# Optimization experiments

Measured on AMD Instinct MI355X. Metric: run time of the kernel, lower is better.

The kernel has to match this reference:

```python
import jax, jax.numpy as jnp
from jax import lax
import numpy as np


def _bn(x, g, b, eps=1e-5):
    # BatchNorm2d in training mode: biased batch stats over (N,H,W) per channel
    m = jnp.mean(x, axis=(0, 2, 3), keepdims=True)
    v = jnp.mean((x - m) ** 2, axis=(0, 2, 3), keepdims=True)
    return (x - m) * lax.rsqrt(v + eps) * g[None, :, None, None] + b[None, :, None, None]


def _conv(x, w, b, pad):
    y = lax.conv_general_dilated(x, w, (1, 1), [(pad, pad), (pad, pad)],
                                 dimension_numbers=('NCHW', 'OIHW', 'NCHW'))
    return y + b[None, :, None, None]


def _prelu(x, a):
    return jnp.where(x >= 0, x, a * x)


def _maxpool2(x):
    return lax.reduce_window(x, -jnp.inf, lax.max, (1, 1, 2, 2), (1, 1, 2, 2), 'VALID')


def _up2(x):
    # UpsamplingBilinear2d(scale_factor=2) -> bilinear, align_corners=True
    B, C, H, W = x.shape
    def idx(n):
        pos = jnp.arange(2 * n, dtype=x.dtype) * (n - 1) / (2 * n - 1)
        lo = jnp.floor(pos).astype(jnp.int32)
        hi = jnp.minimum(lo + 1, n - 1)
        return lo, hi, pos - lo.astype(x.dtype)
    lo, hi, f = idx(H)
    x = x[:, :, lo, :] * (1 - f)[:, None] + x[:, :, hi, :] * f[:, None]
    lo, hi, f = idx(W)
    x = x[:, :, :, lo] * (1 - f) + x[:, :, :, hi] * f
    return x


def _forward(x, n16, sigma16, bias16, prelu_a,
             bn3_g, bn3_b, bn32_g, bn32_b, bn64_g, bn64_b, bn128_g, bn128_b,
             w1, b1, w2, b2, w3, b3, w4, b4, w5, b5, w6, b6, w7, b7, w11, b11):
    B, C, H, W = x.shape
    # 16 enhancement curves fused: r_k = x^{n_k} / (x^{n_k} + sigma_k^{n_k} + bias_k)
    xn = x[None] ** n16[:, None, None, None, None]          # (16,B,3,H,W)
    r = xn / (xn + (sigma16 ** n16)[:, None, None, None, None]
              + bias16[:, None, None, None, None])
    # each branch gets its own BatchNorm2d(3) stats (same affine params)
    r = jax.vmap(lambda t: _bn(t, bn3_g, bn3_b))(r)
    x_fusion = jnp.transpose(r, (1, 0, 2, 3, 4)).reshape(B, 16 * C, H, W)
    x1 = _bn(_maxpool2(_prelu(_conv(x_fusion, w1, b1, 1), prelu_a)), bn32_g, bn32_b)
    x2 = _bn(_maxpool2(_prelu(_conv(x1, w2, b2, 1), prelu_a)), bn64_g, bn64_b)
    x3 = _bn(_maxpool2(_prelu(_conv(x2, w3, b3, 1), prelu_a)), bn128_g, bn128_b)
    x4 = _bn(_conv(x3, w4, b4, 1), bn128_g, bn128_b)
    x5 = _bn(_up2(_prelu(_conv(jnp.concatenate([x4, x3], 1), w5, b5, 1), prelu_a)), bn64_g, bn64_b)
    x6 = _bn(_up2(_prelu(_conv(jnp.concatenate([x2, x5], 1), w6, b6, 1), prelu_a)), bn32_g, bn32_b)
    x_out = jax.nn.sigmoid(_up2(_prelu(_conv(jnp.concatenate([x1, x6], 1), w7, b7, 1), prelu_a)))
    x_out = _conv(x_out, w11, b11, 0)
    x_mean = jnp.mean(x, axis=1, keepdims=True)
    x_out1 = jnp.mean(x_out, axis=1, keepdims=True)
    return x_out1 * (x / (x_mean + 1e-6))


def setup_inputs() -> dict:
    key = jax.random.key(0)
    ks = jax.random.split(key, 16)
    B, H, W = 8, 256, 256
    nf = 32
    x = jax.random.uniform(ks[0], (B, 3, H, W), jnp.float32, 1e-3, 1.0)
    n16 = jnp.arange(1, 17, dtype=jnp.float32) * 0.5
    sigma16 = jnp.full((16,), 0.5, jnp.float32)
    bias16 = jnp.full((16,), 1e-4, jnp.float32)
    prelu_a = jnp.float32(0.25)
    def cw(k, o, i, kk):
        return jax.random.normal(k, (o, i, kk, kk), jnp.float32) * 0.05
    def cb(o):
        return jnp.zeros((o,), jnp.float32)
    return dict(
        x=x, n16=n16, sigma16=sigma16, bias16=bias16, prelu_a=prelu_a,
        bn3_g=jnp.ones((3,), jnp.float32), bn3_b=jnp.zeros((3,), jnp.float32),
        bn32_g=jnp.ones((32,), jnp.float32), bn32_b=jnp.zeros((32,), jnp.float32),
        bn64_g=jnp.ones((64,), jnp.float32), bn64_b=jnp.zeros((64,), jnp.float32),
        bn128_g=jnp.ones((128,), jnp.float32), bn128_b=jnp.zeros((128,), jnp.float32),
        w1=cw(ks[1], nf, 48, 3), b1=cb(nf),
        w2=cw(ks[2], 2 * nf, nf, 3), b2=cb(2 * nf),
        w3=cw(ks[3], 4 * nf, 2 * nf, 3), b3=cb(4 * nf),
        w4=cw(ks[4], 4 * nf, 4 * nf, 3), b4=cb(4 * nf),
        w5=cw(ks[5], 2 * nf, 8 * nf, 3), b5=cb(2 * nf),
        w6=cw(ks[6], nf, 4 * nf, 3), b6=cb(nf),
        w7=cw(ks[7], nf, 2 * nf, 3), b7=cb(nf),
        w11=cw(ks[8], 3, nf, 1), b11=cb(3),
    )


def reference(x, n16, sigma16, bias16, prelu_a,
              bn3_g, bn3_b, bn32_g, bn32_b, bn64_g, bn64_b, bn128_g, bn128_b,
              w1, b1, w2, b2, w3, b3, w4, b4, w5, b5, w6, b6, w7, b7, w11, b11):
    return _forward(x, n16, sigma16, bias16, prelu_a,
                    bn3_g, bn3_b, bn32_g, bn32_b, bn64_g, bn64_b, bn128_g, bn128_b,
                    w1, b1, w2, b2, w3, b3, w4, b4, w5, b5, w6, b6, w7, b7, w11, b11)
```

## Files before the change

kernel.cpp:

```cpp
#include <hip/hip_runtime.h>

#define FAST_EXP2(x) __builtin_amdgcn_exp2f(x)
#define FAST_LOG2(x) __builtin_amdgcn_logf(x)
#define FAST_RCP(x)  __builtin_amdgcn_rcpf(x)

static constexpr size_t S3_SUM=0,   S3_SQ=48;
static constexpr size_t S32A_SUM=96,  S32A_SQ=128;
static constexpr size_t S64A_SUM=160, S64A_SQ=224;
static constexpr size_t S128A_SUM=288,S128A_SQ=416;
static constexpr size_t S128B_SUM=544,S128B_SQ=672;
static constexpr size_t S64B_SUM=800, S64B_SQ=864;
static constexpr size_t S32B_SUM=928, S32B_SQ=960;
static constexpr size_t A3_=1024,  B3_=1072;
static constexpr size_t A32A_=1120, B32A_=1152;
static constexpr size_t A64A_=1184, B64A_=1248;
static constexpr size_t A128A_=1312,B128A_=1440;
static constexpr size_t A128B_=1568,B128B_=1696;
static constexpr size_t A64B_=1824, B64B_=1888;
static constexpr size_t A32B_=1952, B32B_=1984;
static constexpr size_t SPB_=2016, WBAR_=2032, BBAR_=2064;
static constexpr size_t T1_=4096;
static constexpr size_t T2_=T1_+4194304;
static constexpr size_t T3_=T2_+2097152;
static constexpr size_t T4_=T3_+1048576;
static constexpr size_t C5_=T4_+1048576;
static constexpr size_t U5_=C5_+524288;
static constexpr size_t C6_=U5_+2097152;
static constexpr size_t U6_=C6_+1048576;
static constexpr size_t C7_=U6_+4194304;

__global__ void k_precomp(const float* __restrict__ n16, const float* __restrict__ sig16,
                          const float* __restrict__ b16, const float* __restrict__ w11,
                          const float* __restrict__ b11,
                          float* __restrict__ spb, float* __restrict__ wbar, float* __restrict__ bbar)
{
    int t = threadIdx.x;
    if (t < 16) spb[t] = powf(sig16[t], n16[t]) + b16[t];
    else if (t < 48) { int j = t - 16; wbar[j] = (w11[j] + w11[32 + j] + w11[64 + j]) * (1.f/3.f); }
    else if (t == 48) bbar[0] = (b11[0] + b11[1] + b11[2]) * (1.f/3.f);
}

__global__ __launch_bounds__(256) void k_branch_stats(
    const float* __restrict__ x, const float* __restrict__ n16,
    const float* __restrict__ sig16, const float* __restrict__ b16,
    float* __restrict__ sum, float* __restrict__ sq)
{
    const int c = blockIdx.x >> 6;
    const int chunk = blockIdx.x & 63;
    float nk[16], den[16];
#pragma unroll
    for (int k = 0; k < 16; ++k) { nk[k] = n16[k]; den[k] = powf(sig16[k], nk[k]) + b16[k]; }
    float s[16], q[16];
#pragma unroll
    for (int k = 0; k < 16; ++k) { s[k] = 0.f; q[k] = 0.f; }
    const int per = 8192;
    int start = chunk * per;
    for (int i = start + (int)threadIdx.x; i < start + per; i += 256) {
        int b = i >> 16, hw = i & 65535;
        float xv = x[(size_t)(b*3 + c)*65536 + hw];
        float t = FAST_LOG2(xv);
#pragma unroll
        for (int k = 0; k < 16; ++k) {
            float v = FAST_EXP2(nk[k]*t);
            float r = v * FAST_RCP(v + den[k]);
            s[k] += r; q[k] += r*r;
        }
    }
    __shared__ float red[4][32];
    int lane = threadIdx.x & 63, wid = threadIdx.x >> 6;
#pragma unroll
    for (int k = 0; k < 16; ++k) {
#pragma unroll
        for (int off = 32; off > 0; off >>= 1) {
            s[k] += __shfl_down(s[k], off);
            q[k] += __shfl_down(q[k], off);
        }
    }
    if (lane == 0) {
#pragma unroll
        for (int k = 0; k < 16; ++k) { red[wid][k] = s[k]; red[wid][16+k] = q[k]; }
    }
    __syncthreads();
    if (threadIdx.x < 32) {
        float v = red[0][threadIdx.x] + red[1][threadIdx.x] + red[2][threadIdx.x] + red[3][threadIdx.x];
        int k = threadIdx.x & 15;
        if (threadIdx.x < 16) atomicAdd(&sum[k*3 + c], v);
        else                  atomicAdd(&sq[k*3 + c], v);
    }
}

__global__ __launch_bounds__(256) void k_stats(
    const float* __restrict__ in, int C, int HW, int nchunks, int per,
    float* __restrict__ sum, float* __restrict__ sq)
{
    int c = blockIdx.x / nchunks;
    int chunk = blockIdx.x - c*nchunks;
    float s = 0.f, q = 0.f;
    int start = chunk * per, end = start + per;
    for (int i = start + (int)threadIdx.x; i < end; i += 256) {
        int b = i / HW, hw = i - b*HW;
        float v = in[((size_t)b*C + c)*HW + hw];
        s += v; q += v*v;
    }
#pragma unroll
    for (int off = 32; off > 0; off >>= 1) { s += __shfl_down(s, off); q += __shfl_down(q, off); }
    __shared__ float ss[4], qq[4];
    int lane = threadIdx.x & 63, wid = threadIdx.x >> 6;
    if (lane == 0) { ss[wid] = s; qq[wid] = q; }
    __syncthreads();
    if (threadIdx.x == 0) {
        atomicAdd(&sum[c], ss[0]+ss[1]+ss[2]+ss[3]);
        atomicAdd(&sq[c],  qq[0]+qq[1]+qq[2]+qq[3]);
    }
}

__global__ void k_finalize(const float* __restrict__ sum, const float* __restrict__ sq,
                           const float* __restrict__ g, const float* __restrict__ bb,
                           int C, int gdim, float invN,
                           float* __restrict__ A, float* __restrict__ Bs)
{
    int i = blockIdx.x*blockDim.x + threadIdx.x;
    if (i < C) {
        float m   = sum[i]*invN;
        float var = fmaxf(sq[i]*invN - m*m, 0.f);
        float inv = rsqrtf(var + 1e-5f);
        float a   = g[i % gdim]*inv;
        A[i]  = a;
        Bs[i] = bb[i % gdim] - m*a;
    }
}

__global__ __launch_bounds__(256) void k_fill(
    float* __restrict__ out, const float* __restrict__ bias, int C, int HW, int total)
{
    int idx = blockIdx.x*256 + threadIdx.x;
    if (idx < total) {
        int c = (idx / HW) % C;
        out[idx] = bias[c];
    }
}

template<int COG>
__device__ inline void stats_reduce8(float (&ssum)[COG], float (&ssq)[COG],
                                     float (*redst)[16], int cob,
                                     float* __restrict__ gsum, float* __restrict__ gsq)
{
    int lane = threadIdx.x & 63, wid = threadIdx.x >> 6;
#pragma unroll
    for (int co = 0; co < COG; ++co) {
#pragma unroll
        for (int off = 32; off > 0; off >>= 1) {
            ssum[co] += __shfl_down(ssum[co], off);
            ssq[co]  += __shfl_down(ssq[co],  off);
        }
    }
    if (lane == 0) {
#pragma unroll
        for (int co = 0; co < COG; ++co) { redst[wid][co] = ssum[co]; redst[wid][8+co] = ssq[co]; }
    }
    __syncthreads();
    if (threadIdx.x < 16) {
        float v = redst[0][threadIdx.x] + redst[1][threadIdx.x] + redst[2][threadIdx.x] + redst[3][threadIdx.x];
        if (threadIdx.x < 8) atomicAdd(&gsum[cob + threadIdx.x], v);
        else                 atomicAdd(&gsq[cob + threadIdx.x - 8], v);
    }
}

template<int COG>
__global__ __launch_bounds__(256,2) void k_conv1f(
    const float* __restrict__ x,
    const float* __restrict__ n16, const float* __restrict__ spb,
    const float* __restrict__ A, const float* __restrict__ Bs,
    const float* __restrict__ w, const float* __restrict__ bias,
    const float* __restrict__ prelu_a,
    float* __restrict__ out, float* __restrict__ gsum, float* __restrict__ gsq)
{
    const int tx = threadIdx.x & 15, ty = threadIdx.x >> 4;
    const int nco = 32 / COG;
    const int b = blockIdx.z / nco, cob = (blockIdx.z - b*nco)*COG;
    const int x0 = blockIdx.x*32, y0 = blockIdx.y*32;

    __shared__ float wl[COG*48*9];
    __shared__ float rl[3*1224];
    __shared__ float al[48], bl[48], nl[16], dl[16];
    __shared__ float redst[4][16];

    for (int t = threadIdx.x; t < COG*48*9; t += 256) {
        int co = t % COG; int rest = t / COG;
        int kk = rest % 9; int ci = rest / 9;
        wl[t] = w[(((size_t)(cob+co))*48 + ci)*9 + kk];
    }
    if (threadIdx.x < 48) { al[threadIdx.x] = A[threadIdx.x]; bl[threadIdx.x] = Bs[threadIdx.x]; }
    else if (threadIdx.x < 64)  nl[threadIdx.x-48] = n16[threadIdx.x-48];
    else if (threadIdx.x < 80)  dl[threadIdx.x-64] = spb[threadIdx.x-64];

    float tlr[14];
    int off_[14]; int chpack = 0; int okf = 0;
#pragma unroll
    for (int j = 0; j < 14; ++j) {
        int i = threadIdx.x + 256*j;
        if (i < 3468) {
            int ch = i / 1156, jj = i - ch*1156;
            int rr = jj / 34, cc = jj - rr*34;
            int gy = y0 - 1 + rr, gx = x0 - 1 + cc;
            bool ok = (unsigned)gy < 256u && (unsigned)gx < 256u;
            off_[j] = ch*1224 + rr*36 + cc;
            chpack |= ch << (2*j);
            tlr[j] = 0.f;
            if (ok) {
                okf |= 1 << j;
                tlr[j] = FAST_LOG2(x[((size_t)(b*3+ch))*65536 + gy*256 + gx]);
            }
        } else { off_[j] = 3671; tlr[j] = 0.f; }
    }

    float acc[COG][4];
#pragma unroll
    for (int i = 0; i < COG; ++i)
#pragma unroll
        for (int j = 0; j < 4; ++j) acc[i][j] = 0.f;

#pragma unroll 1
    for (int k = 0; k < 16; ++k) {
        __syncthreads();
        float nk = nl[k], dk = dl[k];
#pragma unroll
        for (int j = 0; j < 14; ++j) {
            float rv = 0.f;
            if (okf & (1 << j)) {
                int ch = (chpack >> (2*j)) & 3;
                int chg = k*3 + ch;
                float v = FAST_EXP2(nk * tlr[j]);
                rv = v * FAST_RCP(v + dk) * al[chg] + bl[chg];
            }
            rl[off_[j]] = rv;
        }
        __syncthreads();
#pragma unroll
        for (int ch = 0; ch < 3; ++ch) {
            const float* tlp = &rl[ch*1224 + (2*ty)*36 + 2*tx];
            float iv[4][4];
#pragma unroll
            for (int r = 0; r < 4; ++r) {
                float2 a2 = *(const float2*)(tlp + r*36);
                float2 b2 = *(const float2*)(tlp + r*36 + 2);
                iv[r][0]=a2.x; iv[r][1]=a2.y; iv[r][2]=b2.x; iv[r][3]=b2.y;
            }
            const float* wbase = &wl[((k*3+ch)*9)*COG];
#pragma unroll
            for (int kh = 0; kh < 3; ++kh)
#pragma unroll
            for (int kw = 0; kw < 3; ++kw) {
                const int kk = kh*3 + kw;
                float wv[COG];
#pragma unroll
                for (int q = 0; q < COG/4; ++q) {
                    float4 wq = *((const float4*)(wbase + kk*COG) + q);
                    wv[4*q+0]=wq.x; wv[4*q+1]=wq.y; wv[4*q+2]=wq.z; wv[4*q+3]=wq.w;
                }
#pragma unroll
                for (int co = 0; co < COG; ++co)
#pragma unroll
                    for (int py = 0; py < 2; ++py)
#pragma unroll
                        for (int px = 0; px < 2; ++px)
                            acc[co][py*2+px] += wv[co]*iv[py+kh][px+kw];
            }
        }
    }

    float a = __ldg(prelu_a);
    int pyp = (y0 >> 1) + ty, pxp = (x0 >> 1) + tx;
    float ssum[COG], ssq[COG];
#pragma unroll
    for (int co = 0; co < COG; ++co) {
        float bv = bias[cob + co];
        float v0 = acc[co][0] + bv, v1 = acc[co][1] + bv;
        float v2 = acc[co][2] + bv, v3 = acc[co][3] + bv;
        v0 = v0 >= 0.f ? v0 : a*v0; v1 = v1 >= 0.f ? v1 : a*v1;
        v2 = v2 >= 0.f ? v2 : a*v2; v3 = v3 >= 0.f ? v3 : a*v3;
        float m = fmaxf(fmaxf(v0,v1), fmaxf(v2,v3));
        out[(((size_t)b*32 + cob + co)*128 + pyp)*128 + pxp] = m;
        ssum[co] = m; ssq[co] = m*m;
    }
    __syncthreads();
    stats_reduce8<COG>(ssum, ssq, redst, cob, gsum, gsq);
}

template<int COG, bool POOL>
__global__ __launch_bounds__(256,2) void k_conv_big(
    const float* __restrict__ in1, int C1,
    const float* __restrict__ sc1, const float* __restrict__ sh1,
    const float* __restrict__ w, const float* __restrict__ bias,
    int Cout, int H, int W, const float* __restrict__ prelu_a, int do_prelu,
    float* __restrict__ out, float* __restrict__ gsum, float* __restrict__ gsq)
{
    const int Cin = C1;
    const int tx = threadIdx.x & 15, ty = threadIdx.x >> 4;
    const int nco = Cout / COG;
    const int b = blockIdx.z / nco, cob = (blockIdx.z - b*nco)*COG;
    const int x0 = blockIdx.x*64, y0 = blockIdx.y*32;

    __shared__ float wl[COG*64*9];
    __shared__ float tile[2][34*68];
    __shared__ float redst[4][16];

    for (int t = threadIdx.x; t < COG*Cin*9; t += 256) {
        int co = t % COG; int rest = t / COG;
        int k = rest % 9; int ci = rest / 9;
        wl[t] = w[(((size_t)(cob+co))*Cin + ci)*9 + k];
    }

    float acc[COG][8];
#pragma unroll
    for (int i = 0; i < COG; ++i)
#pragma unroll
        for (int j = 0; j < 8; ++j) acc[i][j] = 0.f;

#pragma unroll 1
    for (int cb = 0; cb < Cin; cb += 2) {
#pragma unroll
        for (int sub = 0; sub < 2; ++sub) {
            int ci = cb + sub;
            float scv = sc1 ? sc1[ci] : 1.f;
            float shv = sc1 ? sh1[ci] : 0.f;
            const float* base = in1 + ((size_t)b*Cin + ci)*H*W;
#pragma unroll 1
            for (int i = threadIdx.x; i < 34*66; i += 256) {
                int r = i / 66, c = i - r*66;
                int gy = y0 - 1 + r, gx = x0 - 1 + c;
                float v = 0.f;
                if ((unsigned)gy < (unsigned)H && (unsigned)gx < (unsigned)W)
                    v = base[(size_t)gy*W + gx]*scv + shv;
                tile[sub][r*68 + c] = v;
            }
        }
        __syncthreads();
#pragma unroll
        for (int sub = 0; sub < 2; ++sub) {
            const float* tl = &tile[sub][(2*ty)*68 + 4*tx];
            float iv[4][6];
#pragma unroll
            for (int r = 0; r < 4; ++r) {
                float4 av = *(const float4*)(tl + r*68);
                float2 bv = *(const float2*)(tl + r*68 + 4);
                iv[r][0]=av.x; iv[r][1]=av.y; iv[r][2]=av.z; iv[r][3]=av.w;
                iv[r][4]=bv.x; iv[r][5]=bv.y;
            }
            const float* wbase = &wl[(cb+sub)*9*COG];
#pragma unroll
            for (int kh = 0; kh < 3; ++kh)
#pragma unroll
            for (int kw = 0; kw < 3; ++kw) {
                const int k = kh*3 + kw;
                float wv[COG];
#pragma unroll
                for (int q = 0; q < COG/4; ++q) {
                    float4 wq = *((const float4*)(wbase + k*COG) + q);
                    wv[4*q+0]=wq.x; wv[4*q+1]=wq.y; wv[4*q+2]=wq.z; wv[4*q+3]=wq.w;
                }
#pragma unroll
                for (int co = 0; co < COG; ++co)
#pragma unroll
                    for (int py = 0; py < 2; ++py)
#pragma unroll
                        for (int px = 0; px < 4; ++px)
                            acc[co][py*4+px] += wv[co]*iv[py+kh][px+kw];
            }
        }
        __syncthreads();
    }

    float a = __ldg(prelu_a);
    float ssum[COG], ssq[COG];
    if (POOL) {
        const int Hp = H >> 1, Wp = W >> 1;
        int pyp = (y0 >> 1) + ty, pxp = (x0 >> 1) + 2*tx;
#pragma unroll
        for (int co = 0; co < COG; ++co) {
            float bv = bias[cob + co];
            float v[8];
#pragma unroll
            for (int p = 0; p < 8; ++p) {
                float t = acc[co][p] + bv;
                v[p] = t >= 0.f ? t : a*t;
            }
            float2 st;
            st.x = fmaxf(fmaxf(v[0], v[1]), fmaxf(v[4], v[5]));
            st.y = fmaxf(fmaxf(v[2], v[3]), fmaxf(v[6], v[7]));
            *(float2*)(out + (((size_t)b*Cout + cob + co)*Hp + pyp)*Wp + pxp) = st;
            ssum[co] = st.x + st.y; ssq[co] = st.x*st.x + st.y*st.y;
        }
        stats_reduce8<COG>(ssum, ssq, redst, cob, gsum, gsq);
    } else {
        int oy = y0 + 2*ty, ox = x0 + 4*tx;
#pragma unroll
        for (int co = 0; co < COG; ++co) {
            float bv = bias[cob + co];
            float* op = out + (((size_t)b*Cout + cob + co)*H + oy)*W + ox;
#pragma unroll
            for (int py = 0; py < 2; ++py) {
                float4 st;
                float t0 = acc[co][py*4+0] + bv, t1 = acc[co][py*4+1] + bv;
                float t2 = acc[co][py*4+2] + bv, t3 = acc[co][py*4+3] + bv;
                if (do_prelu) {
                    t0 = t0 >= 0.f ? t0 : a*t0; t1 = t1 >= 0.f ? t1 : a*t1;
                    t2 = t2 >= 0.f ? t2 : a*t2; t3 = t3 >= 0.f ? t3 : a*t3;
                }
                st.x=t0; st.y=t1; st.z=t2; st.w=t3;
                *(float4*)(op + py*W) = st;
            }
        }
    }
}

template<int COG, int MAXCI, bool POOL, bool SPLIT, bool STATS>
__global__ __launch_bounds__(256,2) void k_conv32(
    const float* __restrict__ in1, int C1,
    const float* __restrict__ sc1, const float* __restrict__ sh1,
    const float* __restrict__ in2, int C2,
    const float* __restrict__ sc2, const float* __restrict__ sh2,
    const float* __restrict__ w, const float* __restrict__ bias,
    int Cout, int H, int W, const float* __restrict__ prelu_a, int do_prelu,
    int ciN, int nsplit,
    float* __restrict__ out, float* __restrict__ gsum, float* __restrict__ gsq)
{
    const int Cin = C1 + C2;
    const int tx = threadIdx.x & 15, ty = threadIdx.x >> 4;
    const int nco = Cout / COG;
    int z = blockIdx.z;
    const int sp = z % nsplit; z /= nsplit;
    const int b = z / nco, cob = (z - b*nco)*COG;
    const int ci0 = sp * ciN;
    const int x0 = blockIdx.x*32, y0 = blockIdx.y*32;

    __shared__ float wl[COG*MAXCI*9];
    __shared__ float tile[2][34*36];
    __shared__ float redst[4][16];

    for (int t = threadIdx.x; t < COG*ciN*9; t += 256) {
        int co = t % COG; int rest = t / COG;
        int k = rest % 9; int ci = rest / 9;
        wl[t] = w[(((size_t)(cob+co))*Cin + ci0 + ci)*9 + k];
    }

    float acc[COG][4];
#pragma unroll
    for (int i = 0; i < COG; ++i)
#pragma unroll
        for (int j = 0; j < 4; ++j) acc[i][j] = 0.f;

#pragma unroll 1
    for (int cb = 0; cb < ciN; cb += 2) {
#pragma unroll
        for (int sub = 0; sub < 2; ++sub) {
            int ci = ci0 + cb + sub;
            const float* in; int cc; const float* scp; const float* shp; int Cn;
            if (ci < C1) { in = in1; cc = ci;      scp = sc1; shp = sh1; Cn = C1; }
            else         { in = in2; cc = ci - C1; scp = sc2; shp = sh2; Cn = C2; }
            float scv = scp ? scp[cc] : 1.f;
            float shv = scp ? shp[cc] : 0.f;
            const float* base = in + ((size_t)b*Cn + cc)*H*W;
#pragma unroll 1
            for (int i = threadIdx.x; i < 34*34; i += 256) {
                int r = i / 34, c = i - r*34;
                int gy = y0 - 1 + r, gx = x0 - 1 + c;
                float v = 0.f;
                if ((unsigned)gy < (unsigned)H && (unsigned)gx < (unsigned)W)
                    v = base[(size_t)gy*W + gx]*scv + shv;
                tile[sub][r*36 + c] = v;
            }
        }
        __syncthreads();
#pragma unroll
        for (int sub = 0; sub < 2; ++sub) {
            const float* tl = &tile[sub][(2*ty)*36 + 2*tx];
            float iv[4][4];
#pragma unroll
            for (int r = 0; r < 4; ++r) {
                float2 a2 = *(const float2*)(tl + r*36);
                float2 b2 = *(const float2*)(tl + r*36 + 2);
                iv[r][0]=a2.x; iv[r][1]=a2.y; iv[r][2]=b2.x; iv[r][3]=b2.y;
            }
            const float* wbase = &wl[(cb+sub)*9*COG];
#pragma unroll
            for (int kh = 0; kh < 3; ++kh)
#pragma unroll
            for (int kw = 0; kw < 3; ++kw) {
                const int k = kh*3 + kw;
                float wv[COG];
#pragma unroll
                for (int q = 0; q < COG/4; ++q) {
                    float4 wq = *((const float4*)(wbase + k*COG) + q);
                    wv[4*q+0]=wq.x; wv[4*q+1]=wq.y; wv[4*q+2]=wq.z; wv[4*q+3]=wq.w;
                }
#pragma unroll
                for (int co = 0; co < COG; ++co)
#pragma unroll
                    for (int py = 0; py < 2; ++py)
#pragma unroll
                        for (int px = 0; px < 2; ++px)
                            acc[co][py*2+px] += wv[co]*iv[py+kh][px+kw];
            }
        }
        __syncthreads();
    }

    if (SPLIT) {
        int oy = y0 + 2*ty, ox = x0 + 2*tx;
#pragma unroll
        for (int co = 0; co < COG; ++co) {
            float* op = out + (((size_t)b*Cout + cob + co)*H + oy)*W + ox;
            atomicAdd(&op[0],     acc[co][0]);
            atomicAdd(&op[1],     acc[co][1]);
            atomicAdd(&op[W],     acc[co][2]);
            atomicAdd(&op[W + 1], acc[co][3]);
        }
    } else {
        float a = __ldg(prelu_a);
        float ssum[COG], ssq[COG];
        if (POOL) {
            const int Hp = H >> 1, Wp = W >> 1;
            int pyp = (y0 >> 1) + ty, pxp = (x0 >> 1) + tx;
#pragma unroll
            for (int co = 0; co < COG; ++co) {
                float bv = bias[cob + co];
                float v0 = acc[co][0] + bv, v1 = acc[co][1] + bv;
                float v2 = acc[co][2] + bv, v3 = acc[co][3] + bv;
                v0 = v0 >= 0.f ? v0 : a*v0; v1 = v1 >= 0.f ? v1 : a*v1;
                v2 = v2 >= 0.f ? v2 : a*v2; v3 = v3 >= 0.f ? v3 : a*v3;
                float m = fmaxf(fmaxf(v0,v1), fmaxf(v2,v3));
                out[(((size_t)b*Cout + cob + co)*Hp + pyp)*Wp + pxp] = m;
                ssum[co] = m; ssq[co] = m*m;
            }
            if (STATS) stats_reduce8<COG>(ssum, ssq, redst, cob, gsum, gsq);
        } else {
            int oy = y0 + 2*ty, ox = x0 + 2*tx;
#pragma unroll
            for (int co = 0; co < COG; ++co) {
                float bv = bias[cob + co];
                float* op = out + (((size_t)b*Cout + cob + co)*H + oy)*W + ox;
                float v0 = acc[co][0] + bv, v1 = acc[co][1] + bv;
                float v2 = acc[co][2] + bv, v3 = acc[co][3] + bv;
                if (do_prelu) {
                    v0 = v0 >= 0.f ? v0 : a*v0; v1 = v1 >= 0.f ? v1 : a*v1;
                    v2 = v2 >= 0.f ? v2 : a*v2; v3 = v3 >= 0.f ? v3 : a*v3;
                }
                op[0] = v0; op[1] = v1; op[W] = v2; op[W+1] = v3;
                ssum[co] = v0+v1+v2+v3; ssq[co] = v0*v0+v1*v1+v2*v2+v3*v3;
            }
            if (STATS) stats_reduce8<COG>(ssum, ssq, redst, cob, gsum, gsq);
        }
    }
}

__global__ __launch_bounds__(256) void k_up2(
    const float* __restrict__ in, float* __restrict__ out, int C, int h, int w,
    const float* __restrict__ prelu_a, int do_prelu,
    float* __restrict__ gsum, float* __restrict__ gsq)
{
    int idx = blockIdx.x*256 + threadIdx.x;
    int W2 = 2*w, H2 = 2*h;
    float a = do_prelu ? __ldg(prelu_a) : 0.f;
    int ox = idx % W2; int t = idx / W2; int oy = t % H2; int bc = t / H2;
    float py = ((float)oy * (float)(h-1)) / (float)(2*h - 1);
    int ly = (int)floorf(py); int hy = min(ly+1, h-1); float fy = py - (float)ly;
    float px = ((float)ox * (float)(w-1)) / (float)(2*w - 1);
    int lx = (int)floorf(px); int hx = min(lx+1, w-1); float fx = px - (float)lx;
    const float* p = in + (size_t)bc*h*w;
    float v00 = p[(size_t)ly*w + lx], v01 = p[(size_t)ly*w + hx];
    float v10 = p[(size_t)hy*w + lx], v11 = p[(size_t)hy*w + hx];
    if (do_prelu) {
        v00 = v00 >= 0.f ? v00 : a*v00;
        v01 = v01 >= 0.f ? v01 : a*v01;
        v10 = v10 >= 0.f ? v10 : a*v10;
        v11 = v11 >= 0.f ? v11 : a*v11;
    }
    float v0 = v00*(1.f-fx) + v01*fx;
    float v1 = v10*(1.f-fx) + v11*fx;
    float v = v0*(1.f-fy) + v1*fy;
    out[idx] = v;
    float s = v, q = v*v;
#pragma unroll
    for (int off = 32; off > 0; off >>= 1) { s += __shfl_down(s, off); q += __shfl_down(q, off); }
    __shared__ float ss[4], qq[4];
    int lane = threadIdx.x & 63, wid = threadIdx.x >> 6;
    if (lane == 0) { ss[wid] = s; qq[wid] = q; }
    __syncthreads();
    if (threadIdx.x == 0) {
        int c = bc % C;
        atomicAdd(&gsum[c], ss[0]+ss[1]+ss[2]+ss[3]);
        atomicAdd(&gsq[c],  qq[0]+qq[1]+qq[2]+qq[3]);
    }
}

__global__ __launch_bounds__(256) void k_final(
    const float* __restrict__ c7, const float* __restrict__ x,
    const float* __restrict__ wbar, const float* __restrict__ bbar,
    float* __restrict__ out)
{
    int idx = blockIdx.x*256 + threadIdx.x;
    if (idx >= 8*65536) return;
    int hw = idx & 65535, b = idx >> 16;
    int oy = hw >> 8, ox = hw & 255;
    float py = ((float)oy * 127.f) / 255.f;
    int ly = (int)floorf(py); int hy = min(ly+1, 127); float fy = py - (float)ly;
    float px = ((float)ox * 127.f) / 255.f;
    int lx = (int)floorf(px); int hx = min(lx+1, 127); float fx = px - (float)lx;
    float w00 = (1.f-fy)*(1.f-fx), w01 = (1.f-fy)*fx, w10 = fy*(1.f-fx), w11v = fy*fx;
    const float* base = c7 + (size_t)b*32*16384;
    float accum = bbar[0];
#pragma unroll 8
    for (int j = 0; j < 32; ++j) {
        const float* p = base + (size_t)j*16384;
        float v = p[ly*128 + lx]*w00 + p[ly*128 + hx]*w01 + p[hy*128 + lx]*w10 + p[hy*128 + hx]*w11v;
        float s = FAST_RCP(1.f + __expf(-v));
        accum += wbar[j]*s;
    }
    size_t xb = (size_t)b*3*65536 + hw;
    float x0 = x[xb], x1 = x[xb + 65536], x2 = x[xb + 2*65536];
    float m = (x0 + x1 + x2)*(1.f/3.f) + 1e-6f;
    float sc = accum * FAST_RCP(m);
    out[xb]            = sc*x0;
    out[xb + 65536]    = sc*x1;
    out[xb + 2*65536]  = sc*x2;
}

extern "C" void kernel_launch(void* const* d_in, const int* in_sizes, int n_in,
                              void* d_out, int out_size, void* d_ws, size_t ws_size,
                              hipStream_t stream) {
    const float* x       = (const float*)d_in[0];
    const float* n16     = (const float*)d_in[1];
    const float* sig16   = (const float*)d_in[2];
    const float* bia16   = (const float*)d_in[3];
    const float* prelu_a = (const float*)d_in[4];
    const float* bn3_g   = (const float*)d_in[5];
    const float* bn3_b   = (const float*)d_in[6];
    const float* bn32_g  = (const float*)d_in[7];
    const float* bn32_b  = (const float*)d_in[8];
    const float* bn64_g  = (const float*)d_in[9];
    const float* bn64_b  = (const float*)d_in[10];
    const float* bn128_g = (const float*)d_in[11];
    const float* bn128_b = (const float*)d_in[12];
    const float* w1 = (const float*)d_in[13]; const float* b1 = (const float*)d_in[14];
    const float* w2 = (const float*)d_in[15]; const float* b2 = (const float*)d_in[16];
    const float* w3 = (const float*)d_in[17]; const float* b3 = (const float*)d_in[18];
    const float* w4 = (const float*)d_in[19]; const float* b4 = (const float*)d_in[20];
    const float* w5 = (const float*)d_in[21]; const float* b5 = (const float*)d_in[22];
    const float* w6 = (const float*)d_in[23]; const float* b6 = (const float*)d_in[24];
    const float* w7 = (const float*)d_in[25]; const float* b7 = (const float*)d_in[26];
    const float* w11= (const float*)d_in[27]; const float* b11= (const float*)d_in[28];
    float* ws  = (float*)d_ws;
    float* out = (float*)d_out;

    (void)hipMemsetAsync(d_ws, 0, 4096*sizeof(float), stream);

    k_precomp<<<1, 64, 0, stream>>>(n16, sig16, bia16, w11, b11, ws+SPB_, ws+WBAR_, ws+BBAR_);

    k_branch_stats<<<192, 256, 0, stream>>>(x, n16, sig16, bia16, ws+S3_SUM, ws+S3_SQ);
    k_finalize<<<1, 128, 0, stream>>>(ws+S3_SUM, ws+S3_SQ, bn3_g, bn3_b, 48, 3, 1.f/524288.f, ws+A3_, ws+B3_);

    k_conv1f<8><<<dim3(8,8,32), 256, 0, stream>>>(x, n16, ws+SPB_, ws+A3_, ws+B3_,
                                                  w1, b1, prelu_a, ws+T1_, ws+S32A_SUM, ws+S32A_SQ);
    k_finalize<<<1, 128, 0, stream>>>(ws+S32A_SUM, ws+S32A_SQ, bn32_g, bn32_b, 32, 32, 1.f/131072.f, ws+A32A_, ws+B32A_);

    k_conv_big<8,true><<<dim3(2,4,64), 256, 0, stream>>>(
        ws+T1_, 32, ws+A32A_, ws+B32A_, w2, b2, 64, 128, 128, prelu_a, 1,
        ws+T2_, ws+S64A_SUM, ws+S64A_SQ);
    k_finalize<<<1, 128, 0, stream>>>(ws+S64A_SUM, ws+S64A_SQ, bn64_g, bn64_b, 64, 64, 1.f/32768.f, ws+A64A_, ws+B64A_);

    k_conv32<8,64,true,false,true><<<dim3(2,2,128), 256, 0, stream>>>(
        ws+T2_, 64, ws+A64A_, ws+B64A_, nullptr, 0, nullptr, nullptr,
        w3, b3, 128, 64, 64, prelu_a, 1, 64, 1, ws+T3_, ws+S128A_SUM, ws+S128A_SQ);
    k_finalize<<<1, 128, 0, stream>>>(ws+S128A_SUM, ws+S128A_SQ, bn128_g, bn128_b, 128, 128, 1.f/8192.f, ws+A128A_, ws+B128A_);

    k_fill<<<4096, 256, 0, stream>>>(ws+T4_, b4, 128, 1024, 1048576);
    k_conv32<8,32,false,true,false><<<dim3(1,1,512), 256, 0, stream>>>(
        ws+T3_, 128, ws+A128A_, ws+B128A_, nullptr, 0, nullptr, nullptr,
        w4, nullptr, 128, 32, 32, prelu_a, 0, 32, 4, ws+T4_, nullptr, nullptr);
    k_stats<<<512, 256, 0, stream>>>(ws+T4_, 128, 1024, 4, 2048, ws+S128B_SUM, ws+S128B_SQ);
    k_finalize<<<1, 128, 0, stream>>>(ws+S128B_SUM, ws+S128B_SQ, bn128_g, bn128_b, 128, 128, 1.f/8192.f, ws+A128B_, ws+B128B_);

    k_fill<<<2048, 256, 0, stream>>>(ws+C5_, b5, 64, 1024, 524288);
    k_conv32<8,32,false,true,false><<<dim3(1,1,512), 256, 0, stream>>>(
        ws+T4_, 128, ws+A128B_, ws+B128B_, ws+T3_, 128, ws+A128A_, ws+B128A_,
        w5, nullptr, 64, 32, 32, prelu_a, 0, 32, 8, ws+C5_, nullptr, nullptr);
    k_up2<<<8192, 256, 0, stream>>>(ws+C5_, ws+U5_, 64, 32, 32, prelu_a, 1, ws+S64B_SUM, ws+S64B_SQ);
    k_finalize<<<1, 128, 0, stream>>>(ws+S64B_SUM, ws+S64B_SQ, bn64_g, bn64_b, 64, 64, 1.f/32768.f, ws+A64B_, ws+B64B_);

    k_fill<<<4096, 256, 0, stream>>>(ws+C6_, b6, 32, 4096, 1048576);
    k_conv32<8,32,false,true,false><<<dim3(2,2,128), 256, 0, stream>>>(
        ws+T2_, 64, ws+A64A_, ws+B64A_, ws+U5_, 64, ws+A64B_, ws+B64B_,
        w6, nullptr, 32, 64, 64, prelu_a, 0, 32, 4, ws+C6_, nullptr, nullptr);
    k_up2<<<16384, 256, 0, stream>>>(ws+C6_, ws+U6_, 32, 64, 64, prelu_a, 1, ws+S32B_SUM, ws+S32B_SQ);
    k_finalize<<<1, 128, 0, stream>>>(ws+S32B_SUM, ws+S32B_SQ, bn32_g, bn32_b, 32, 32, 1.f/131072.f, ws+A32B_, ws+B32B_);

    k_conv32<8,64,false,false,false><<<dim3(4,4,32), 256, 0, stream>>>(
        ws+T1_, 32, ws+A32A_, ws+B32A_, ws+U6_, 32, ws+A32B_, ws+B32B_,
        w7, b7, 32, 128, 128, prelu_a, 1, 64, 1, ws+C7_, nullptr, nullptr);

    k_final<<<2048, 256, 0, stream>>>(ws+C7_, x, ws+WBAR_, ws+BBAR_, out);
}
```

Baseline: 1.398 ms.

## Fold branch BatchNorm into conv1 weights and hoist log inputs into registers

The per-branch BatchNorm affine is folded into the first conv: weights are scaled by A, bias absorbs B, and padded positions take -B/A so that they still produce zero after folding. The conv1 kernel now loads the log of the input tile once into registers and recomputes the curve per k, dropping two block barriers and the shared-memory rewrite in each of the 16 iterations. Separately, each finalize is merged with the following bias fill to remove launches. The risks are more exp/rcp work per thread (16 elements instead of about 14), higher register pressure from 48 extra live values, and precision trouble if A is near zero.

Measured after the change: 1.485 ms. 1.06x slower.

```diff
diff --git a/kernel.cpp b/kernel.cpp
--- a/kernel.cpp
+++ b/kernel.cpp
@@ -28,6 +28,9 @@
 static constexpr size_t C6_=U5_+2097152;
 static constexpr size_t U6_=C6_+1048576;
 static constexpr size_t C7_=U6_+4194304;
+static constexpr size_t W1S_=C7_+4194304;
+static constexpr size_t B1S_=W1S_+13824;
+static constexpr size_t PAD_=B1S_+64;
 
 __global__ void k_precomp(const float* __restrict__ n16, const float* __restrict__ sig16,
                           const float* __restrict__ b16, const float* __restrict__ w11,
@@ -130,13 +133,45 @@
     }
 }
 
-__global__ __launch_bounds__(256) void k_fill(
-    float* __restrict__ out, const float* __restrict__ bias, int C, int HW, int total)
-{
+__global__ __launch_bounds__(256) void k_finalize_fill(
+    const float* __restrict__ sum, const float* __restrict__ sq,
+    const float* __restrict__ g, const float* __restrict__ bb,
+    int C, int gdim, float invN,
+    float* __restrict__ A, float* __restrict__ Bs,
+    const float* __restrict__ fbias, float* __restrict__ fout, int fC, int fHW, int ftotal)
+{
+    if (blockIdx.x == 0 && threadIdx.x < (unsigned)C) {
+        int i = threadIdx.x;
+        float m   = sum[i]*invN;
+        float var = fmaxf(sq[i]*invN - m*m, 0.f);
+        float inv = rsqrtf(var + 1e-5f);
+        float a   = g[i % gdim]*inv;
+        A[i]  = a;
+        Bs[i] = bb[i % gdim] - m*a;
+    }
     int idx = blockIdx.x*256 + threadIdx.x;
-    if (idx < total) {
-        int c = (idx / HW) % C;
-        out[idx] = bias[c];
+    if (idx < ftotal) {
+        int c = (idx / fHW) % fC;
+        fout[idx] = fbias[c];
+    }
+}
+
+__global__ __launch_bounds__(256) void k_prep1(
+    const float* __restrict__ w1, const float* __restrict__ b1,
+    const float* __restrict__ A3, const float* __restrict__ B3,
+    float* __restrict__ w1s, float* __restrict__ b1s, float* __restrict__ padg)
+{
+    int tid = threadIdx.x;
+    for (int t = tid; t < 13824; t += 256) {
+        int ci = (t / 9) % 48;
+        w1s[t] = w1[t] * A3[ci];
+    }
+    if (tid < 48) padg[tid] = -B3[tid] * FAST_RCP(A3[tid]);
+    if (tid < 32) {
+        float s = b1[tid];
+        const float* wp = w1 + tid*432;
+        for (int i = 0; i < 432; ++i) s += wp[i] * B3[i/9];
+        b1s[tid] = s;
     }
 }
 
@@ -170,8 +205,8 @@
 __global__ __launch_bounds__(256,2) void k_conv1f(
     const float* __restrict__ x,
     const float* __restrict__ n16, const float* __restrict__ spb,
-    const float* __restrict__ A, const float* __restrict__ Bs,
-    const float* __restrict__ w, const float* __restrict__ bias,
+    const float* __restrict__ w1s, const float* __restrict__ b1s,
+    const float* __restrict__ padg,
     const float* __restrict__ prelu_a,
     float* __restrict__ out, float* __restrict__ gsum, float* __restrict__ gsq)
 {
@@ -181,21 +216,19 @@
     const int x0 = blockIdx.x*32, y0 = blockIdx.y*32;
 
     __shared__ float wl[COG*48*9];
-    __shared__ float rl[3*1224];
-    __shared__ float al[48], bl[48], nl[16], dl[16];
+    __shared__ float tl[3*1224];
+    __shared__ float nl[16], dl[16], padl[48];
     __shared__ float redst[4][16];
 
     for (int t = threadIdx.x; t < COG*48*9; t += 256) {
         int co = t % COG; int rest = t / COG;
         int kk = rest % 9; int ci = rest / 9;
-        wl[t] = w[(((size_t)(cob+co))*48 + ci)*9 + kk];
-    }
-    if (threadIdx.x < 48) { al[threadIdx.x] = A[threadIdx.x]; bl[threadIdx.x] = Bs[threadIdx.x]; }
-    else if (threadIdx.x < 64)  nl[threadIdx.x-48] = n16[threadIdx.x-48];
-    else if (threadIdx.x < 80)  dl[threadIdx.x-64] = spb[threadIdx.x-64];
-
-    float tlr[14];
-    int off_[14]; int chpack = 0; int okf = 0;
+        wl[t] = w1s[(((size_t)(cob+co))*48 + ci)*9 + kk];
+    }
+    if (threadIdx.x < 16)       nl[threadIdx.x]      = n16[threadIdx.x];
+    else if (threadIdx.x < 32)  dl[threadIdx.x-16]   = spb[threadIdx.x-16];
+    else if (threadIdx.x < 80)  padl[threadIdx.x-32] = padg[threadIdx.x-32];
+
 #pragma unroll
     for (int j = 0; j < 14; ++j) {
         int i = threadIdx.x + 256*j;
@@ -203,16 +236,33 @@
             int ch = i / 1156, jj = i - ch*1156;
             int rr = jj / 34, cc = jj - rr*34;
             int gy = y0 - 1 + rr, gx = x0 - 1 + cc;
-            bool ok = (unsigned)gy < 256u && (unsigned)gx < 256u;
-            off_[j] = ch*1224 + rr*36 + cc;
-            chpack |= ch << (2*j);
-            tlr[j] = 0.f;
-            if (ok) {
-                okf |= 1 << j;
-                tlr[j] = FAST_LOG2(x[((size_t)(b*3+ch))*65536 + gy*256 + gx]);
-            }
-        } else { off_[j] = 3671; tlr[j] = 0.f; }
-    }
+            float tv = 0.f;
+            if ((unsigned)gy < 256u && (unsigned)gx < 256u)
+                tv = FAST_LOG2(x[((size_t)(b*3+ch))*65536 + gy*256 + gx]);
+            tl[ch*1224 + rr*36 + cc] = tv;
+        }
+    }
+    __syncthreads();
+
+    float ivt[3][16];
+#pragma unroll
+    for (int ch = 0; ch < 3; ++ch) {
+        const float* tlp = &tl[ch*1224 + (2*ty)*36 + 2*tx];
+#pragma unroll
+        for (int r = 0; r < 4; ++r) {
+            float2 a2 = *(const float2*)(tlp + r*36);
+            float2 b2 = *(const float2*)(tlp + r*36 + 2);
+            ivt[ch][r*4+0]=a2.x; ivt[ch][r*4+1]=a2.y; ivt[ch][r*4+2]=b2.x; ivt[ch][r*4+3]=b2.y;
+        }
+    }
+    unsigned mask = 0;
+#pragma unroll
+    for (int r = 0; r < 4; ++r)
+#pragma unroll
+        for (int c = 0; c < 4; ++c) {
+            int gy = y0 + 2*ty - 1 + r, gx = x0 + 2*tx - 1 + c;
+            if ((unsigned)gy < 256u && (unsigned)gx < 256u) mask |= 1u << (r*4+c);
+        }
 
     float acc[COG][4];
 #pragma unroll
@@ -222,29 +272,16 @@
 
 #pragma unroll 1
     for (int k = 0; k < 16; ++k) {
-        __syncthreads();
         float nk = nl[k], dk = dl[k];
 #pragma unroll
-        for (int j = 0; j < 14; ++j) {
-            float rv = 0.f;
-            if (okf & (1 << j)) {
-                int ch = (chpack >> (2*j)) & 3;
-                int chg = k*3 + ch;
-                float v = FAST_EXP2(nk * tlr[j]);
-                rv = v * FAST_RCP(v + dk) * al[chg] + bl[chg];
-            }
-            rl[off_[j]] = rv;
-        }
-        __syncthreads();
-#pragma unroll
         for (int ch = 0; ch < 3; ++ch) {
-            const float* tlp = &rl[ch*1224 + (2*ty)*36 + 2*tx];
-            float iv[4][4];
-#pragma unroll
-            for (int r = 0; r < 4; ++r) {
-                float2 a2 = *(const float2*)(tlp + r*36);
-                float2 b2 = *(const float2*)(tlp + r*36 + 2);
-                iv[r][0]=a2.x; iv[r][1]=a2.y; iv[r][2]=b2.x; iv[r][3]=b2.y;
+            float pv = padl[k*3 + ch];
+            float rr_[16];
+#pragma unroll
+            for (int e = 0; e < 16; ++e) {
+                float v = FAST_EXP2(nk * ivt[ch][e]);
+                float rv = v * FAST_RCP(v + dk);
+                rr_[e] = ((mask >> e) & 1u) ? rv : pv;
             }
             const float* wbase = &wl[((k*3+ch)*9)*COG];
 #pragma unroll
@@ -264,7 +301,7 @@
                     for (int py = 0; py < 2; ++py)
 #pragma unroll
                         for (int px = 0; px < 2; ++px)
-                            acc[co][py*2+px] += wv[co]*iv[py+kh][px+kw];
+                            acc[co][py*2+px] += wv[co]*rr_[(py+kh)*4 + (px+kw)];
             }
         }
     }
@@ -274,7 +311,7 @@
     float ssum[COG], ssq[COG];
 #pragma unroll
     for (int co = 0; co < COG; ++co) {
-        float bv = bias[cob + co];
+        float bv = b1s[cob + co];
         float v0 = acc[co][0] + bv, v1 = acc[co][1] + bv;
         float v2 = acc[co][2] + bv, v3 = acc[co][3] + bv;
         v0 = v0 >= 0.f ? v0 : a*v0; v1 = v1 >= 0.f ? v1 : a*v1;
@@ -659,9 +696,10 @@
 
     k_branch_stats<<<192, 256, 0, stream>>>(x, n16, sig16, bia16, ws+S3_SUM, ws+S3_SQ);
     k_finalize<<<1, 128, 0, stream>>>(ws+S3_SUM, ws+S3_SQ, bn3_g, bn3_b, 48, 3, 1.f/524288.f, ws+A3_, ws+B3_);
-
-    k_conv1f<8><<<dim3(8,8,32), 256, 0, stream>>>(x, n16, ws+SPB_, ws+A3_, ws+B3_,
-                                                  w1, b1, prelu_a, ws+T1_, ws+S32A_SUM, ws+S32A_SQ);
+    k_prep1<<<1, 256, 0, stream>>>(w1, b1, ws+A3_, ws+B3_, ws+W1S_, ws+B1S_, ws+PAD_);
+
+    k_conv1f<8><<<dim3(8,8,32), 256, 0, stream>>>(x, n16, ws+SPB_, ws+W1S_, ws+B1S_, ws+PAD_,
+                                                  prelu_a, ws+T1_, ws+S32A_SUM, ws+S32A_SQ);
     k_finalize<<<1, 128, 0, stream>>>(ws+S32A_SUM, ws+S32A_SQ, bn32_g, bn32_b, 32, 32, 1.f/131072.f, ws+A32A_, ws+B32A_);
 
     k_conv_big<8,true><<<dim3(2,4,64), 256, 0, stream>>>(
@@ -672,23 +710,26 @@
     k_conv32<8,64,true,false,true><<<dim3(2,2,128), 256, 0, stream>>>(
         ws+T2_, 64, ws+A64A_, ws+B64A_, nullptr, 0, nullptr, nullptr,
         w3, b3, 128, 64, 64, prelu_a, 1, 64, 1, ws+T3_, ws+S128A_SUM, ws+S128A_SQ);
-    k_finalize<<<1, 128, 0, stream>>>(ws+S128A_SUM, ws+S128A_SQ, bn128_g, bn128_b, 128, 128, 1.f/8192.f, ws+A128A_, ws+B128A_);
-
-    k_fill<<<4096, 256, 0, stream>>>(ws+T4_, b4, 128, 1024, 1048576);
+    k_finalize_fill<<<4096, 256, 0, stream>>>(ws+S128A_SUM, ws+S128A_SQ, bn128_g, bn128_b,
+                                              128, 128, 1.f/8192.f, ws+A128A_, ws+B128A_,
+                                              b4, ws+T4_, 128, 1024, 1048576);
+
     k_conv32<8,32,false,true,false><<<dim3(1,1,512), 256, 0, stream>>>(
         ws+T3_, 128, ws+A128A_, ws+B128A_, nullptr, 0, nullptr, nullptr,
         w4, nullptr, 128, 32, 32, prelu_a, 0, 32, 4, ws+T4_, nullptr, nullptr);
     k_stats<<<512, 256, 0, stream>>>(ws+T4_, 128, 1024, 4, 2048, ws+S128B_SUM, ws+S128B_SQ);
-    k_finalize<<<1, 128, 0, stream>>>(ws+S128B_SUM, ws+S128B_SQ, bn128_g, bn128_b, 128, 128, 1.f/8192.f, ws+A128B_, ws+B128B_);
-
-    k_fill<<<2048, 256, 0, stream>>>(ws+C5_, b5, 64, 1024, 524288);
+    k_finalize_fill<<<2048, 256, 0, stream>>>(ws+S128B_SUM, ws+S128B_SQ, bn128_g, bn128_b,
+                                              128, 128, 1.f/8192.f, ws+A128B_, ws+B128B_,
+                                              b5, ws+C5_, 64, 1024, 524288);
+
     k_conv32<8,32,false,true,false><<<dim3(1,1,512), 256, 0, stream>>>(
         ws+T4_, 128, ws+A128B_, ws+B128B_, ws+T3_, 128, ws+A128A_, ws+B128A_,
         w5, nullptr, 64, 32, 32, prelu_a, 0, 32, 8, ws+C5_, nullptr, nullptr);
     k_up2<<<8192, 256, 0, stream>>>(ws+C5_, ws+U5_, 64, 32, 32, prelu_a, 1, ws+S64B_SUM, ws+S64B_SQ);
-    k_finalize<<<1, 128, 0, stream>>>(ws+S64B_SUM, ws+S64B_SQ, bn64_g, bn64_b, 64, 64, 1.f/32768.f, ws+A64B_, ws+B64B_);
-
-    k_fill<<<4096, 256, 0, stream>>>(ws+C6_, b6, 32, 4096, 1048576);
+    k_finalize_fill<<<4096, 256, 0, stream>>>(ws+S64B_SUM, ws+S64B_SQ, bn64_g, bn64_b,
+                                              64, 64, 1.f/32768.f, ws+A64B_, ws+B64B_,
+                                              b6, ws+C6_, 32, 4096, 1048576);
+
     k_conv32<8,32,false,true,false><<<dim3(2,2,128), 256, 0, stream>>>(
         ws+T2_, 64, ws+A64A_, ws+B64A_, ws+U5_, 64, ws+A64B_, ws+B64B_,
         w6, nullptr, 32, 64, 64, prelu_a, 0, 32, 4, ws+C6_, nullptr, nullptr);
```
